# Kernel tuning notes

Measured on AMD Instinct MI355X. Metric: run time of the kernel, lower is better.

## Reference

```python
import jax, jax.numpy as jnp
import numpy as np

B, S, D, N, R = 4, 2048, 1024, 64, 128

def setup_inputs() -> dict:
    key = jax.random.key(0)
    k1, k2, k3, k4, k5 = jax.random.split(key, 5)
    x = jax.random.normal(k1, (B, S, D), dtype=jnp.float32)
    feature_know_w = jax.random.uniform(k2, (B, S, N), dtype=jnp.float32)
    restore_know_w = jax.random.uniform(k3, (B, S, N), dtype=jnp.float32)
    # neuron pools, scaled like typical init
    feature_know = jax.random.normal(k4, (N, D, R), dtype=jnp.float32) / np.sqrt(D)
    restore_know = jax.random.normal(k5, (N, R, D), dtype=jnp.float32) / np.sqrt(R)
    return {"x": x, "feature_know_w": feature_know_w, "restore_know_w": restore_know_w,
            "feature_know": feature_know, "restore_know": restore_know}

def reference(x, feature_know_w, restore_know_w, feature_know, restore_know):
    # Feature stage: all_h[b,s,n,r] = sum_d x[b,s,d] * feature_know[n,d,r];
    # h[b,s,r] = sum_n all_h[b,s,n,r] * feature_know_w[b,s,n].
    # Fused into one einsum (same math, XLA picks pairwise contraction;
    # largest intermediate is [B,S,N,R], never [B,S,N,D]).
    h = jnp.einsum('bsd,ndr,bsn->bsr', x, feature_know, feature_know_w)
    # Restore stage: all_out[b,s,n,d] = sum_r h[b,s,r] * restore_know[n,r,d];
    # out[b,s,d] = sum_n all_out[b,s,n,d] * restore_know_w[b,s,n].
    # Reordered contraction keeps the intermediate at [B,S,N,R] instead of [B,S,N,D].
    out = jnp.einsum('bsr,bsn,nrd->bsd', h, restore_know_w, restore_know)
    # dropout p=0.0 -> identity
    return out
```

## Files before the change

### kernel.cpp

```cpp
#include <hip/hip_runtime.h>
#include <stdint.h>


typedef unsigned short ushort_t;
typedef __attribute__((ext_vector_type(8))) short frag_t;
typedef __attribute__((ext_vector_type(4))) float f32x4;

#define BK 64

__device__ __forceinline__ unsigned short f2bf(float f) {
    unsigned int u = __builtin_bit_cast(unsigned int, f);
    u = (u + 0x7FFFu + ((u >> 16) & 1u)) >> 16;
    return (unsigned short)u;
}

__device__ __forceinline__ void glds16(const ushort_t* g, ushort_t* l) {
    __builtin_amdgcn_global_load_lds(
        (const __attribute__((address_space(1))) unsigned int*)g,
        (__attribute__((address_space(3))) unsigned int*)l,
        16, 0, 0);
}

__global__ __launch_bounds__(256) void convert_bf(const float* __restrict__ in,
                                                  ushort_t* __restrict__ out, int n8) {
    int idx = blockIdx.x * 256 + threadIdx.x;
    if (idx >= n8) return;
    const float4 v0 = ((const float4*)in)[idx * 2];
    const float4 v1 = ((const float4*)in)[idx * 2 + 1];
    unsigned short b[8] = { f2bf(v0.x), f2bf(v0.y), f2bf(v0.z), f2bf(v0.w),
                            f2bf(v1.x), f2bf(v1.y), f2bf(v1.z), f2bf(v1.w) };
    ((uint4*)out)[idx] = *(const uint4*)b;
}

__global__ __launch_bounds__(256) void transpose_bf(const float* __restrict__ in,
                                                    ushort_t* __restrict__ out,
                                                    int R, int C) {
    __shared__ float tile[64][65];
    const int t  = threadIdx.x;
    const int r0 = blockIdx.x * 64;
    const int c0 = blockIdx.y * 64;
    const int ci = t & 63;
    const int rb = t >> 6;
    #pragma unroll
    for (int p = 0; p < 16; ++p)
        tile[rb + 4 * p][ci] = in[(size_t)(r0 + rb + 4 * p) * C + c0 + ci];
    __syncthreads();
    const int cw = t >> 2;
    const int rg = (t & 3) * 16;
    unsigned short buf[16];
    #pragma unroll
    for (int k = 0; k < 16; ++k)
        buf[k] = f2bf(tile[rg + k][cw]);
    uint4* dst = (uint4*)&out[(size_t)(c0 + cw) * R + r0 + rg];
    dst[0] = *(const uint4*)&buf[0];
    dst[1] = *(const uint4*)&buf[8];
}

template<int SHIFT, int SEG_STEPS, bool ATOMIC>
__global__ __launch_bounds__(256, 4)
void kc_gemm(const ushort_t* __restrict__ Ab, const float* __restrict__ W,
             const ushort_t* __restrict__ Bt, float* __restrict__ C,
             int ldA, int ldB, int ldC, int ksteps)
{
    __shared__ ushort_t As[64 * BK];
    __shared__ ushort_t Bs[128 * BK];

    const int t    = threadIdx.x;
    const int lane = t & 63;
    const int wv   = t >> 6;
    const int m0   = blockIdx.x * 64;
    const int n0   = blockIdx.y * 128;
    const int kbase = blockIdx.z * ksteps * BK;

    const int wm = (wv & 1) * 32;
    const int wn = (wv >> 1) * 64;
    const int fr = lane & 15;
    const int q  = lane >> 4;
    const int e  = fr & 7;

    int arow[2], acol[2];
    #pragma unroll
    for (int c = 0; c < 2; ++c) {
        const int s = (wv * 2 + c) * 64 + lane;
        arow[c] = s >> 3;
        acol[c] = ((s & 7) ^ (arow[c] & 7)) * 8;
    }
    int brow[4], bcol[4];
    #pragma unroll
    for (int c = 0; c < 4; ++c) {
        const int s = (wv * 4 + c) * 64 + lane;
        brow[c] = s >> 3;
        bcol[c] = ((s & 7) ^ (brow[c] & 7)) * 8;
    }

    f32x4 acc_out[2][4];
    #pragma unroll
    for (int i = 0; i < 2; ++i)
        #pragma unroll
        for (int j = 0; j < 4; ++j)
            acc_out[i][j] = (f32x4){0.f, 0.f, 0.f, 0.f};

    const int nsegs = ksteps / SEG_STEPS;
    for (int seg = 0; seg < nsegs; ++seg) {
        const int segk = kbase + seg * SEG_STEPS * BK;
        const int nidx = segk >> SHIFT;

        f32x4 acc_in[2][4];
        #pragma unroll
        for (int i = 0; i < 2; ++i)
            #pragma unroll
            for (int j = 0; j < 4; ++j)
                acc_in[i][j] = (f32x4){0.f, 0.f, 0.f, 0.f};

        for (int ss = 0; ss < SEG_STEPS; ++ss) {
            const int k0 = segk + ss * BK;
            const int d0 = k0 & ((1 << SHIFT) - 1);

            __syncthreads();
            #pragma unroll
            for (int c = 0; c < 2; ++c)
                glds16(Ab + (size_t)(m0 + arow[c]) * ldA + d0 + acol[c],
                       &As[(wv * 2 + c) * 512]);
            #pragma unroll
            for (int c = 0; c < 4; ++c)
                glds16(Bt + (size_t)(n0 + brow[c]) * ldB + k0 + bcol[c],
                       &Bs[(wv * 4 + c) * 512]);
            __syncthreads();

            #pragma unroll
            for (int kk = 0; kk < 2; ++kk) {
                const int csw = (kk * 4 + q) ^ e;
                frag_t a[2], b[4];
                #pragma unroll
                for (int i = 0; i < 2; ++i)
                    a[i] = *(const frag_t*)&As[((wm + 16 * i + fr) * 8 + csw) * 8];
                #pragma unroll
                for (int j = 0; j < 4; ++j)
                    b[j] = *(const frag_t*)&Bs[((wn + 16 * j + fr) * 8 + csw) * 8];
                #pragma unroll
                for (int i = 0; i < 2; ++i)
                    #pragma unroll
                    for (int j = 0; j < 4; ++j)
                        acc_in[i][j] = __builtin_amdgcn_mfma_f32_16x16x32_bf16(
                                           a[i], b[j], acc_in[i][j], 0, 0, 0);
            }
        }

        #pragma unroll
        for (int i = 0; i < 2; ++i) {
            #pragma unroll
            for (int r = 0; r < 4; ++r) {
                const int gm = m0 + wm + 16 * i + q * 4 + r;
                const float w = W[(size_t)gm * 64 + nidx];
                #pragma unroll
                for (int j = 0; j < 4; ++j)
                    acc_out[i][j][r] += w * acc_in[i][j][r];
            }
        }
    }

    #pragma unroll
    for (int i = 0; i < 2; ++i) {
        #pragma unroll
        for (int j = 0; j < 4; ++j) {
            #pragma unroll
            for (int r = 0; r < 4; ++r) {
                const int gm = m0 + wm + 16 * i + q * 4 + r;
                const int gn = n0 + wn + 16 * j + fr;
                if constexpr (ATOMIC)
                    atomicAdd(&C[(size_t)gm * ldC + gn], acc_out[i][j][r]);
                else
                    C[(size_t)gm * ldC + gn] = acc_out[i][j][r];
            }
        }
    }
}

extern "C" void kernel_launch(void* const* d_in, const int* in_sizes, int n_in,
                              void* d_out, int out_size, void* d_ws, size_t ws_size,
                              hipStream_t stream) {
    const float* x  = (const float*)d_in[0];
    const float* w1 = (const float*)d_in[1];
    const float* w2 = (const float*)d_in[2];
    const float* F  = (const float*)d_in[3];
    const float* Rk = (const float*)d_in[4];
    float* out = (float*)d_out;

    char* ws = (char*)d_ws;
    float*    h    = (float*)ws;
    ushort_t* buf1 = (ushort_t*)(ws + ((size_t)4  << 20));
    ushort_t* F_t  = (ushort_t*)(ws + ((size_t)20 << 20));
    ushort_t* h_bf = (ushort_t*)(ws + ((size_t)36 << 20));

    hipMemsetAsync(h, 0, (size_t)8192 * 128 * sizeof(float), stream);

    convert_bf<<<4096, 256, 0, stream>>>(x, buf1, 1048576);
    transpose_bf<<<dim3(1024, 2), 256, 0, stream>>>(F, F_t, 65536, 128);

    kc_gemm<10, 16, true><<<dim3(128, 1, 8), 256, 0, stream>>>(
        buf1, w1, F_t, h, 1024, 65536, 128, 128);

    convert_bf<<<512, 256, 0, stream>>>(h, h_bf, 131072);
    transpose_bf<<<dim3(128, 16), 256, 0, stream>>>(Rk, buf1, 8192, 1024);

    kc_gemm<7, 2, false><<<dim3(128, 8, 1), 256, 0, stream>>>(
        h_bf, w2, buf1, out, 128, 8192, 1024, 128);
}
```

Before: 500.4 us.

## Materialize per-neuron projections with large-tile GEMMs and fuse neuron weighting

When the workspace is large enough, computes x·F for all neurons as one 8192x8192 bf16 GEMM with 128x128 tiles, then a small kernel reduces over neurons with w1 and rescales by w2 in place. The result feeds a single K=8192 GEMM against the transposed restore pool. This removes split-K atomics and the per-segment weight fold from the GEMM loops, but adds a large bf16 intermediate written and read through memory. A fallback keeps the old path for small workspaces.

```diff
diff --git a/kernel.cpp b/kernel.cpp
--- a/kernel.cpp
+++ b/kernel.cpp
@@ -12,6 +12,12 @@
     unsigned int u = __builtin_bit_cast(unsigned int, f);
     u = (u + 0x7FFFu + ((u >> 16) & 1u)) >> 16;
     return (unsigned short)u;
+}
+__device__ __forceinline__ float bf2f_lo(unsigned int v) {
+    return __builtin_bit_cast(float, v << 16);
+}
+__device__ __forceinline__ float bf2f_hi(unsigned int v) {
+    return __builtin_bit_cast(float, v & 0xFFFF0000u);
 }
 
 __device__ __forceinline__ void glds16(const ushort_t* g, ushort_t* l) {
@@ -34,8 +40,11 @@
 
 __global__ __launch_bounds__(256) void transpose_bf(const float* __restrict__ in,
                                                     ushort_t* __restrict__ out,
-                                                    int R, int C) {
+                                                    int R, int C,
+                                                    long in_bstride, long out_bstride) {
     __shared__ float tile[64][65];
+    in  += (long)blockIdx.z * in_bstride;
+    out += (long)blockIdx.z * out_bstride;
     const int t  = threadIdx.x;
     const int r0 = blockIdx.x * 64;
     const int c0 = blockIdx.y * 64;
@@ -56,66 +65,156 @@
     dst[1] = *(const uint4*)&buf[8];
 }
 
-template<int SHIFT, int SEG_STEPS, bool ATOMIC>
-__global__ __launch_bounds__(256, 4)
-void kc_gemm(const ushort_t* __restrict__ Ab, const float* __restrict__ W,
-             const ushort_t* __restrict__ Bt, float* __restrict__ C,
-             int ldA, int ldB, int ldC, int ksteps)
+__global__ __launch_bounds__(256) void mid_fuse(ushort_t* __restrict__ y,
+                                                const float* __restrict__ w1,
+                                                const float* __restrict__ w2) {
+    const int m    = blockIdx.x * 4 + (threadIdx.x >> 6);
+    const int lane = threadIdx.x & 63;
+    unsigned int* yrow = (unsigned int*)(y + (size_t)m * 8192);
+    const float* w1r = w1 + (size_t)m * 64;
+    const float* w2r = w2 + (size_t)m * 64;
+    float h0 = 0.f, h1 = 0.f;
+    #pragma unroll 16
+    for (int n = 0; n < 64; ++n) {
+        const unsigned int v = yrow[n * 64 + lane];
+        const float w = w1r[n];
+        h0 += w * bf2f_lo(v);
+        h1 += w * bf2f_hi(v);
+    }
+    #pragma unroll 16
+    for (int n = 0; n < 64; ++n) {
+        const float w = w2r[n];
+        yrow[n * 64 + lane] =
+            (unsigned int)f2bf(w * h0) | ((unsigned int)f2bf(w * h1) << 16);
+    }
+}
+
+template<bool OUT_BF16>
+__global__ __launch_bounds__(256, 3)
+void kc_gemm(const ushort_t* __restrict__ Ab, const ushort_t* __restrict__ Bt,
+             void* __restrict__ Cout, int ldA, int ldB, int ldC, int ksteps)
 {
-    __shared__ ushort_t As[64 * BK];
+    __shared__ ushort_t As[128 * BK];
     __shared__ ushort_t Bs[128 * BK];
 
     const int t    = threadIdx.x;
     const int lane = t & 63;
     const int wv   = t >> 6;
-    const int m0   = blockIdx.x * 64;
+    const int m0   = blockIdx.x * 128;
     const int n0   = blockIdx.y * 128;
-    const int kbase = blockIdx.z * ksteps * BK;
-
-    const int wm = (wv & 1) * 32;
+
+    const int wm = (wv & 1) * 64;
     const int wn = (wv >> 1) * 64;
     const int fr = lane & 15;
     const int q  = lane >> 4;
     const int e  = fr & 7;
 
-    int arow[2], acol[2];
+    int srow[4], scol[4];
+    #pragma unroll
+    for (int c = 0; c < 4; ++c) {
+        const int s = (wv * 4 + c) * 64 + lane;
+        srow[c] = s >> 3;
+        scol[c] = ((s & 7) ^ (srow[c] & 7)) * 8;
+    }
+
+    f32x4 acc[4][4];
+    #pragma unroll
+    for (int i = 0; i < 4; ++i)
+        #pragma unroll
+        for (int j = 0; j < 4; ++j)
+            acc[i][j] = (f32x4){0.f, 0.f, 0.f, 0.f};
+
+    for (int ss = 0; ss < ksteps; ++ss) {
+        const int k0 = ss * BK;
+
+        __syncthreads();
+        #pragma unroll
+        for (int c = 0; c < 4; ++c)
+            glds16(Ab + (size_t)(m0 + srow[c]) * ldA + k0 + scol[c],
+                   &As[(wv * 4 + c) * 512]);
+        #pragma unroll
+        for (int c = 0; c < 4; ++c)
+            glds16(Bt + (size_t)(n0 + srow[c]) * ldB + k0 + scol[c],
+                   &Bs[(wv * 4 + c) * 512]);
+        __syncthreads();
+
+        #pragma unroll
+        for (int kk = 0; kk < 2; ++kk) {
+            const int csw = (kk * 4 + q) ^ e;
+            frag_t a[4], b[4];
+            #pragma unroll
+            for (int i = 0; i < 4; ++i)
+                a[i] = *(const frag_t*)&As[((wm + 16 * i + fr) * 8 + csw) * 8];
+            #pragma unroll
+            for (int j = 0; j < 4; ++j)
+                b[j] = *(const frag_t*)&Bs[((wn + 16 * j + fr) * 8 + csw) * 8];
+            #pragma unroll
+            for (int i = 0; i < 4; ++i)
+                #pragma unroll
+                for (int j = 0; j < 4; ++j)
+                    acc[i][j] = __builtin_amdgcn_mfma_f32_16x16x32_bf16(
+                                    a[i], b[j], acc[i][j], 0, 0, 0);
+        }
+    }
+
+    #pragma unroll
+    for (int i = 0; i < 4; ++i) {
+        #pragma unroll
+        for (int r = 0; r < 4; ++r) {
+            const int gm = m0 + wm + 16 * i + q * 4 + r;
+            #pragma unroll
+            for (int j = 0; j < 4; ++j) {
+                const int gn = n0 + wn + 16 * j + fr;
+                if constexpr (OUT_BF16)
+                    ((ushort_t*)Cout)[(size_t)gm * ldC + gn] = f2bf(acc[i][j][r]);
+                else
+                    ((float*)Cout)[(size_t)gm * ldC + gn] = acc[i][j][r];
+            }
+        }
+    }
+}
+
+template<int SHIFT, int SEG_STEPS, bool ATOMIC>
+__global__ __launch_bounds__(256, 4)
+void kc_gemm_fold(const ushort_t* __restrict__ Ab, const float* __restrict__ W,
+                  const ushort_t* __restrict__ Bt, float* __restrict__ C,
+                  int ldA, int ldB, int ldC, int ksteps)
+{
+    __shared__ ushort_t As[64 * BK];
+    __shared__ ushort_t Bs[128 * BK];
+    const int t = threadIdx.x, lane = t & 63, wv = t >> 6;
+    const int m0 = blockIdx.x * 64, n0 = blockIdx.y * 128;
+    const int kbase = blockIdx.z * ksteps * BK;
+    const int wm = (wv & 1) * 32, wn = (wv >> 1) * 64;
+    const int fr = lane & 15, q = lane >> 4, e = fr & 7;
+    int arow[2], acol[2], brow[4], bcol[4];
     #pragma unroll
     for (int c = 0; c < 2; ++c) {
         const int s = (wv * 2 + c) * 64 + lane;
-        arow[c] = s >> 3;
-        acol[c] = ((s & 7) ^ (arow[c] & 7)) * 8;
-    }
-    int brow[4], bcol[4];
+        arow[c] = s >> 3; acol[c] = ((s & 7) ^ (arow[c] & 7)) * 8;
+    }
     #pragma unroll
     for (int c = 0; c < 4; ++c) {
         const int s = (wv * 4 + c) * 64 + lane;
-        brow[c] = s >> 3;
-        bcol[c] = ((s & 7) ^ (brow[c] & 7)) * 8;
-    }
-
+        brow[c] = s >> 3; bcol[c] = ((s & 7) ^ (brow[c] & 7)) * 8;
+    }
     f32x4 acc_out[2][4];
     #pragma unroll
     for (int i = 0; i < 2; ++i)
         #pragma unroll
-        for (int j = 0; j < 4; ++j)
-            acc_out[i][j] = (f32x4){0.f, 0.f, 0.f, 0.f};
-
+        for (int j = 0; j < 4; ++j) acc_out[i][j] = (f32x4){0.f,0.f,0.f,0.f};
     const int nsegs = ksteps / SEG_STEPS;
     for (int seg = 0; seg < nsegs; ++seg) {
         const int segk = kbase + seg * SEG_STEPS * BK;
         const int nidx = segk >> SHIFT;
-
         f32x4 acc_in[2][4];
         #pragma unroll
         for (int i = 0; i < 2; ++i)
             #pragma unroll
-            for (int j = 0; j < 4; ++j)
-                acc_in[i][j] = (f32x4){0.f, 0.f, 0.f, 0.f};
-
+            for (int j = 0; j < 4; ++j) acc_in[i][j] = (f32x4){0.f,0.f,0.f,0.f};
         for (int ss = 0; ss < SEG_STEPS; ++ss) {
             const int k0 = segk + ss * BK;
             const int d0 = k0 & ((1 << SHIFT) - 1);
-
             __syncthreads();
             #pragma unroll
             for (int c = 0; c < 2; ++c)
@@ -126,17 +225,16 @@
                 glds16(Bt + (size_t)(n0 + brow[c]) * ldB + k0 + bcol[c],
                        &Bs[(wv * 4 + c) * 512]);
             __syncthreads();
-
             #pragma unroll
             for (int kk = 0; kk < 2; ++kk) {
                 const int csw = (kk * 4 + q) ^ e;
                 frag_t a[2], b[4];
                 #pragma unroll
                 for (int i = 0; i < 2; ++i)
-                    a[i] = *(const frag_t*)&As[((wm + 16 * i + fr) * 8 + csw) * 8];
+                    a[i] = *(const frag_t*)&As[((wm + 16*i + fr) * 8 + csw) * 8];
                 #pragma unroll
                 for (int j = 0; j < 4; ++j)
-                    b[j] = *(const frag_t*)&Bs[((wn + 16 * j + fr) * 8 + csw) * 8];
+                    b[j] = *(const frag_t*)&Bs[((wn + 16*j + fr) * 8 + csw) * 8];
                 #pragma unroll
                 for (int i = 0; i < 2; ++i)
                     #pragma unroll
@@ -145,35 +243,27 @@
                                            a[i], b[j], acc_in[i][j], 0, 0, 0);
             }
         }
-
-        #pragma unroll
-        for (int i = 0; i < 2; ++i) {
+        #pragma unroll
+        for (int i = 0; i < 2; ++i)
             #pragma unroll
             for (int r = 0; r < 4; ++r) {
-                const int gm = m0 + wm + 16 * i + q * 4 + r;
+                const int gm = m0 + wm + 16*i + q*4 + r;
                 const float w = W[(size_t)gm * 64 + nidx];
                 #pragma unroll
-                for (int j = 0; j < 4; ++j)
-                    acc_out[i][j][r] += w * acc_in[i][j][r];
+                for (int j = 0; j < 4; ++j) acc_out[i][j][r] += w * acc_in[i][j][r];
             }
-        }
-    }
-
-    #pragma unroll
-    for (int i = 0; i < 2; ++i) {
-        #pragma unroll
-        for (int j = 0; j < 4; ++j) {
+    }
+    #pragma unroll
+    for (int i = 0; i < 2; ++i)
+        #pragma unroll
+        for (int j = 0; j < 4; ++j)
             #pragma unroll
             for (int r = 0; r < 4; ++r) {
-                const int gm = m0 + wm + 16 * i + q * 4 + r;
-                const int gn = n0 + wn + 16 * j + fr;
-                if constexpr (ATOMIC)
-                    atomicAdd(&C[(size_t)gm * ldC + gn], acc_out[i][j][r]);
-                else
-                    C[(size_t)gm * ldC + gn] = acc_out[i][j][r];
+                const int gm = m0 + wm + 16*i + q*4 + r;
+                const int gn = n0 + wn + 16*j + fr;
+                if constexpr (ATOMIC) atomicAdd(&C[(size_t)gm * ldC + gn], acc_out[i][j][r]);
+                else C[(size_t)gm * ldC + gn] = acc_out[i][j][r];
             }
-        }
-    }
 }
 
 extern "C" void kernel_launch(void* const* d_in, const int* in_sizes, int n_in,
@@ -187,22 +277,46 @@
     float* out = (float*)d_out;
 
     char* ws = (char*)d_ws;
-    float*    h    = (float*)ws;
-    ushort_t* buf1 = (ushort_t*)(ws + ((size_t)4  << 20));
-    ushort_t* F_t  = (ushort_t*)(ws + ((size_t)20 << 20));
-    ushort_t* h_bf = (ushort_t*)(ws + ((size_t)36 << 20));
-
-    hipMemsetAsync(h, 0, (size_t)8192 * 128 * sizeof(float), stream);
-
-    convert_bf<<<4096, 256, 0, stream>>>(x, buf1, 1048576);
-    transpose_bf<<<dim3(1024, 2), 256, 0, stream>>>(F, F_t, 65536, 128);
-
-    kc_gemm<10, 16, true><<<dim3(128, 1, 8), 256, 0, stream>>>(
-        buf1, w1, F_t, h, 1024, 65536, 128, 128);
-
-    convert_bf<<<512, 256, 0, stream>>>(h, h_bf, 131072);
-    transpose_bf<<<dim3(128, 16), 256, 0, stream>>>(Rk, buf1, 8192, 1024);
-
-    kc_gemm<7, 2, false><<<dim3(128, 8, 1), 256, 0, stream>>>(
-        h_bf, w2, buf1, out, 128, 8192, 1024, 128);
-}
+    const size_t MB = (size_t)1 << 20;
+
+    if (ws_size >= 160 * MB) {
+        ushort_t* y    = (ushort_t*)ws;
+        ushort_t* x_bf = (ushort_t*)(ws + 128 * MB);
+        ushort_t* F_t2 = (ushort_t*)(ws + 144 * MB);
+        ushort_t* Rk_t = x_bf;
+
+        convert_bf<<<4096, 256, 0, stream>>>(x, x_bf, 1048576);
+        transpose_bf<<<dim3(16, 2, 64), 256, 0, stream>>>(
+            F, F_t2, 1024, 128, 131072, 131072);
+
+        kc_gemm<true><<<dim3(64, 64), 256, 0, stream>>>(
+            x_bf, F_t2, y, 1024, 1024, 8192, 16);
+
+        mid_fuse<<<2048, 256, 0, stream>>>(y, w1, w2);
+
+        transpose_bf<<<dim3(128, 16, 1), 256, 0, stream>>>(
+            Rk, Rk_t, 8192, 1024, 0, 0);
+
+        kc_gemm<false><<<dim3(64, 8), 256, 0, stream>>>(
+            y, Rk_t, out, 8192, 8192, 1024, 128);
+    } else {
+        float*    h    = (float*)ws;
+        ushort_t* x_bf = (ushort_t*)(ws + 4  * MB);
+        ushort_t* Rk_t = (ushort_t*)(ws + 4  * MB);
+        ushort_t* F_t  = (ushort_t*)(ws + 20 * MB);
+        ushort_t* h_bf = (ushort_t*)(ws + 36 * MB);
+
+        hipMemsetAsync(h, 0, 4 * MB, stream);
+        convert_bf<<<4096, 256, 0, stream>>>(x, x_bf, 1048576);
+        transpose_bf<<<dim3(1024, 2, 1), 256, 0, stream>>>(F, F_t, 65536, 128, 0, 0);
+
+        kc_gemm_fold<10, 16, true><<<dim3(128, 1, 8), 256, 0, stream>>>(
+            x_bf, w1, F_t, h, 1024, 65536, 128, 128);
+
+        convert_bf<<<512, 256, 0, stream>>>(h, h_bf, 131072);
+        transpose_bf<<<dim3(128, 16, 1), 256, 0, stream>>>(Rk, Rk_t, 8192, 1024, 0, 0);
+
+        kc_gemm_fold<7, 2, false><<<dim3(128, 8, 1), 256, 0, stream>>>(
+            h_bf, w2, Rk_t, out, 128, 8192, 1024, 128);
+    }
+}
```

New measurement: 456.5 us. 8.8% less time.
